# Kernel optimization log

Measured on AMD Instinct MI355X. Metric: run time of the kernel, lower is better.

Reference implementation:

```python
import jax, jax.numpy as jnp
import numpy as np

EPS = 1e-5
B, C_IN, T_IN = 512, 12, 5000
NF, HID, LAT = 32, 64, 32


def setup_inputs() -> dict:
    key = jax.random.key(0)
    ks = jax.random.split(key, 12)
    inp = {
        "x": jax.random.normal(ks[0], (B, C_IN, T_IN), dtype=jnp.float32),
        # conv stack
        "conv1_w": jax.random.normal(ks[1], (32, C_IN, 50), dtype=jnp.float32) * 0.05,
        "conv1_b": jnp.zeros((32,), dtype=jnp.float32),
        "bn1_g": jnp.ones((32,), dtype=jnp.float32),
        "bn1_b": jnp.zeros((32,), dtype=jnp.float32),
        "conv2_w": jax.random.normal(ks[2], (NF, 32, 25), dtype=jnp.float32) * 0.05,
        "conv2_b": jnp.zeros((NF,), dtype=jnp.float32),
        "bn2_g": jnp.ones((NF,), dtype=jnp.float32),
        "bn2_b": jnp.zeros((NF,), dtype=jnp.float32),
        # input projection + layernorm
        "proj_w": jax.random.normal(ks[3], (LAT, NF), dtype=jnp.float32) * 0.1,
        "proj_b": jnp.zeros((LAT,), dtype=jnp.float32),
        "ln_g": jnp.ones((LAT,), dtype=jnp.float32),
        "ln_b": jnp.zeros((LAT,), dtype=jnp.float32),
        # PLRNN recurrence params
        "A": jnp.eye(LAT, dtype=jnp.float32) * 0.9,
        "W": jax.random.normal(ks[4], (LAT, HID), dtype=jnp.float32) * 0.1,
        "h_bias": jnp.zeros((HID,), dtype=jnp.float32),
        # output projection
        "out_w": jax.random.normal(ks[5], (LAT, LAT), dtype=jnp.float32) * 0.1,
        "out_b": jnp.zeros((LAT,), dtype=jnp.float32),
    }
    return inp


def _conv1d(x, w, b, stride):
    # x: [B, C, T], w: [O, I, K]
    y = jax.lax.conv_general_dilated(
        x, w, window_strides=(stride,), padding="VALID",
        dimension_numbers=("NCH", "OIH", "NCH"))
    return y + b[None, :, None]


def _batchnorm_train(x, g, b):
    # training-mode BN over (batch, time) per channel; x: [B, C, T]
    mean = jnp.mean(x, axis=(0, 2), keepdims=True)
    var = jnp.mean((x - mean) ** 2, axis=(0, 2), keepdims=True)
    return (x - mean) * jax.lax.rsqrt(var + EPS) * g[None, :, None] + b[None, :, None]


def _layernorm(x, g, b):
    mean = jnp.mean(x, axis=-1, keepdims=True)
    var = jnp.mean((x - mean) ** 2, axis=-1, keepdims=True)
    return (x - mean) * jax.lax.rsqrt(var + EPS) * g + b


def reference(x, conv1_w, conv1_b, bn1_g, bn1_b, conv2_w, conv2_b, bn2_g, bn2_b,
              proj_w, proj_b, ln_g, ln_b, A, W, h_bias, out_w, out_b):
    # conv front-end
    y = jax.nn.relu(_batchnorm_train(_conv1d(x, conv1_w, conv1_b, 10), bn1_g, bn1_b))
    y = jax.nn.relu(_batchnorm_train(_conv1d(y, conv2_w, conv2_b, 5), bn2_g, bn2_b))
    y = jnp.transpose(y, (0, 2, 1))  # [B, T, NF], T = 95

    # input projection + LN, vectorized over all timesteps
    xt = _layernorm(jnp.einsum("btf,lf->btl", y, proj_w) + proj_b, ln_g, ln_b)  # [B, T, L]
    xs = jnp.transpose(xt, (1, 0, 2))  # [T, B, L] for scan

    def step(h, x_t):
        # h: [B, L]
        linear = h @ A.T
        nonlinear = jax.nn.relu(h @ W + h_bias) @ W.T
        h_new = linear + nonlinear + x_t
        return h_new, h_new

    h0 = jnp.zeros((x.shape[0], A.shape[0]), dtype=x.dtype)
    _, outputs = jax.lax.scan(step, h0, xs)  # [T, B, L]

    pooled = jnp.mean(outputs, axis=0)  # [B, L]
    return pooled @ out_w.T + out_b
```

## Files before the change

### kernel.cpp

```cpp
#include <hip/hip_runtime.h>

#define NB    512
#define CIN   12
#define TIN   5000
#define C1    32
#define T1    496
#define T2    95
#define LATD  32
#define HIDD  64

#define OFS_STATS 0
#define OFS_W1P   256
#define OFS_W2P   19456
#define OFS_Y1    45056
#define OFS_Y2    8171520
#define OFS_XS    OFS_Y1

__global__ void prep_kernel(const float* __restrict__ w1, const float* __restrict__ w2,
                            float* __restrict__ ws) {
    int idx = blockIdx.x * 256 + threadIdx.x;
    if (idx < 256) ws[idx] = 0.f;
    int j = idx - 256;
    if (j >= 0 && j < 19200) {
        int ic = j / 1600, r = j % 1600;
        int p = r / 160, rr = r % 160, jj = rr / 32, oc = rr % 32;
        ws[OFS_W1P + j] = w1[oc * 600 + ic * 50 + 10 * jj + p];
    }
    int j2 = idx - 19456;
    if (j2 >= 0 && j2 < 25600) {
        int ic = j2 / 800, r = j2 % 800;
        int p = r / 160, rr = r % 160, jj = rr / 32, oc = rr % 32;
        ws[OFS_W2P + j2] = w2[oc * 800 + ic * 25 + 5 * jj + p];
    }
}

__global__ __launch_bounds__(256, 4) void conv1_kernel(const float* __restrict__ x,
                                                       const float* __restrict__ b1,
                                                       float* __restrict__ ws) {
    const float* w1p = ws + OFS_W1P;
    float* y1 = ws + OFS_Y1;
    float* stats = ws + OFS_STATS;
    int b  = blockIdx.x >> 1;
    int t0 = (blockIdx.x & 1) * 256;
    int tid = threadIdx.x;
    int ocg = tid & 7, tg = tid >> 3;
    int oc0 = ocg * 4, lt0 = tg * 8;

    __shared__ __align__(16) float xs_s[2][2680];
    __shared__ __align__(16) float ws_s[2][1600];
    __shared__ float sred[256];

    float acc[4][8];
#pragma unroll
    for (int a = 0; a < 4; ++a)
#pragma unroll
        for (int c = 0; c < 8; ++c) acc[a][c] = 0.f;

    const float* xb = x + (size_t)b * (CIN * TIN) + t0 * 10;
    int nvalid = TIN - t0 * 10;

    float4 px[3];
    float4 pw[2];

    auto fetch = [&](int ic) {
#pragma unroll
        for (int j = 0; j < 3; ++j) {
            int i = tid + j * 256;
            if (i < 650) {
                int src = 4 * i;
                const float* gp = xb + ic * TIN + src;
                float4 v;
                if (src + 4 <= nvalid) {
                    v = *(const float4*)gp;
                } else {
                    v.x = (src + 0 < nvalid) ? gp[0] : 0.f;
                    v.y = (src + 1 < nvalid) ? gp[1] : 0.f;
                    v.z = (src + 2 < nvalid) ? gp[2] : 0.f;
                    v.w = (src + 3 < nvalid) ? gp[3] : 0.f;
                }
                px[j] = v;
            }
        }
#pragma unroll
        for (int j = 0; j < 2; ++j) {
            int i = tid + j * 256;
            if (i < 400) pw[j] = *(const float4*)(w1p + ic * 1600 + 4 * i);
        }
    };

    auto stage = [&](int cur) {
#pragma unroll
        for (int j = 0; j < 3; ++j) {
            int i = tid + j * 256;
            if (i < 650) {
                int g = 4 * i;
                int col = g / 10, p = g - 10 * col;
                float vals[4] = {px[j].x, px[j].y, px[j].z, px[j].w};
#pragma unroll
                for (int m = 0; m < 4; ++m) {
                    int pm = p + m;
                    int rr = (pm >= 10) ? pm - 10 : pm;
                    int cc = col + ((pm >= 10) ? 1 : 0);
                    xs_s[cur][rr * 268 + cc] = vals[m];
                }
            }
        }
#pragma unroll
        for (int j = 0; j < 2; ++j) {
            int i = tid + j * 256;
            if (i < 400) *(float4*)&ws_s[cur][4 * i] = pw[j];
        }
    };

    fetch(0);
    stage(0);
    fetch(1);
    __syncthreads();

    for (int ic = 0; ic < CIN; ++ic) {
        int cur = ic & 1;
        if (ic + 1 < CIN) stage(cur ^ 1);
        if (ic + 2 < CIN) fetch(ic + 2);

#pragma unroll 2
        for (int p = 0; p < 10; ++p) {
            const float* xr = &xs_s[cur][p * 268 + 8 * tg];
            float4 xa = *(const float4*)(xr);
            float4 xbv = *(const float4*)(xr + 4);
            float4 xc = *(const float4*)(xr + 8);
            float xv[12] = {xa.x, xa.y, xa.z, xa.w,
                            xbv.x, xbv.y, xbv.z, xbv.w,
                            xc.x, xc.y, xc.z, xc.w};
            const float* wr = &ws_s[cur][p * 160 + oc0];
            float4 w0 = *(const float4*)(wr);
            float4 w1v = *(const float4*)(wr + 32);
            float4 w2v = *(const float4*)(wr + 64);
            float4 w3v = *(const float4*)(wr + 96);
            float4 w4v = *(const float4*)(wr + 128);
            float wj[5][4] = {{w0.x, w0.y, w0.z, w0.w},
                              {w1v.x, w1v.y, w1v.z, w1v.w},
                              {w2v.x, w2v.y, w2v.z, w2v.w},
                              {w3v.x, w3v.y, w3v.z, w3v.w},
                              {w4v.x, w4v.y, w4v.z, w4v.w}};
#pragma unroll
            for (int j = 0; j < 5; ++j)
#pragma unroll
                for (int jt = 0; jt < 8; ++jt) {
                    float xx = xv[jt + j];
#pragma unroll
                    for (int jo = 0; jo < 4; ++jo)
                        acc[jo][jt] = fmaf(wj[j][jo], xx, acc[jo][jt]);
                }
        }
        __syncthreads();
    }

    float bias[4];
#pragma unroll
    for (int jo = 0; jo < 4; ++jo) bias[jo] = b1[oc0 + jo];

    bool tvalid = (t0 + lt0) <= (T1 - 8);
    float psum[4], psq[4];
#pragma unroll
    for (int jo = 0; jo < 4; ++jo) {
        float s = 0.f, q = 0.f;
        if (tvalid) {
            float tmp[8];
#pragma unroll
            for (int jt = 0; jt < 8; ++jt) {
                float v = acc[jo][jt] + bias[jo];
                tmp[jt] = v; s += v; q = fmaf(v, v, q);
            }
            float* yrow = y1 + (size_t)(b * 32 + oc0 + jo) * T1 + t0 + lt0;
            float4 o0; o0.x = tmp[0]; o0.y = tmp[1]; o0.z = tmp[2]; o0.w = tmp[3];
            float4 o1; o1.x = tmp[4]; o1.y = tmp[5]; o1.z = tmp[6]; o1.w = tmp[7];
            *(float4*)yrow       = o0;
            *(float4*)(yrow + 4) = o1;
        }
        psum[jo] = s; psq[jo] = q;
    }
#pragma unroll
    for (int off = 32; off >= 8; off >>= 1) {
#pragma unroll
        for (int jo = 0; jo < 4; ++jo) {
            psum[jo] += __shfl_down(psum[jo], off, 64);
            psq[jo]  += __shfl_down(psq[jo],  off, 64);
        }
    }
    int lane = tid & 63, wvi = tid >> 6;
    if (lane < 8) {
#pragma unroll
        for (int jo = 0; jo < 4; ++jo) {
            sred[((wvi * 8 + lane) * 4 + jo) * 2 + 0] = psum[jo];
            sred[((wvi * 8 + lane) * 4 + jo) * 2 + 1] = psq[jo];
        }
    }
    __syncthreads();
    if (tid < 64) {
        int oc = tid >> 1, which = tid & 1;
        int og = oc >> 2, jo = oc & 3;
        float v = 0.f;
#pragma unroll
        for (int w = 0; w < 4; ++w)
            v += sred[((w * 8 + og) * 4 + jo) * 2 + which];
        atomicAdd(&stats[which * 32 + oc], v);
    }
}

__global__ __launch_bounds__(384, 2) void conv2_kernel(const float* __restrict__ b2,
                                                       const float* __restrict__ g1,
                                                       const float* __restrict__ be1,
                                                       float* __restrict__ ws) {
    const float* w2p = ws + OFS_W2P;
    const float* y1 = ws + OFS_Y1;
    float* y2 = ws + OFS_Y2;
    float* stats = ws + OFS_STATS;
    int b = blockIdx.x;
    int tid = threadIdx.x;
    int hf = (tid >= 192) ? 1 : 0;
    int ltid = tid - hf * 192;
    int icbase = hf * 16;
    int ocg = ltid & 7, tg = ltid >> 3;
    int oc0 = ocg * 4, lt0 = tg * 4;

    __shared__ __align__(16) float a1s[2][2][500];
    __shared__ __align__(16) float w2s[2][2][800];
    __shared__ __align__(16) float comb[16 * 192];
    __shared__ float sred[192];
    __shared__ float bns[64];

    if (tid < 32) {
        float mean = stats[tid] * (1.f / 253952.f);
        float var  = stats[32 + tid] * (1.f / 253952.f) - mean * mean;
        float s = g1[tid] * rsqrtf(var + 1e-5f);
        bns[tid]      = s;
        bns[32 + tid] = be1[tid] - mean * s;
    }

    float acc[4][4];
#pragma unroll
    for (int a = 0; a < 4; ++a)
#pragma unroll
        for (int c = 0; c < 4; ++c) acc[a][c] = 0.f;

    float4 py, pw0, pw1;
    auto fetch = [&](int k) {
        int ic = icbase + k;
        const float* yrow = y1 + (size_t)(b * 32 + ic) * T1;
        if (ltid < 124) py = *(const float4*)(yrow + 4 * ltid);
        pw0 = *(const float4*)(w2p + ic * 800 + 4 * ltid);
        if (ltid < 8) pw1 = *(const float4*)(w2p + ic * 800 + 4 * (ltid + 192));
    };

    auto stage = [&](int k, int cur) {
        int ic = icbase + k;
        if (ltid < 124) {
            float s1 = bns[ic], sh1 = bns[32 + ic];
            float vals[4];
            vals[0] = fmaxf(fmaf(py.x, s1, sh1), 0.f);
            vals[1] = fmaxf(fmaf(py.y, s1, sh1), 0.f);
            vals[2] = fmaxf(fmaf(py.z, s1, sh1), 0.f);
            vals[3] = fmaxf(fmaf(py.w, s1, sh1), 0.f);
            int g = 4 * ltid;
            int col = g / 5, p = g - 5 * col;
#pragma unroll
            for (int m = 0; m < 4; ++m) {
                int pm = p + m;
                int rr = (pm >= 5) ? pm - 5 : pm;
                int cc = col + ((pm >= 5) ? 1 : 0);
                a1s[hf][cur][rr * 100 + cc] = vals[m];
            }
        }
        *(float4*)&w2s[hf][cur][4 * ltid] = pw0;
        if (ltid < 8) *(float4*)&w2s[hf][cur][4 * (ltid + 192)] = pw1;
    };

    fetch(0);
    __syncthreads();
    stage(0, 0);
    fetch(1);
    __syncthreads();

    for (int k = 0; k < 16; ++k) {
        int cur = k & 1;
        if (k + 1 < 16) stage(k + 1, cur ^ 1);
        if (k + 2 < 16) fetch(k + 2);

#pragma unroll 2
        for (int p = 0; p < 5; ++p) {
            const float* xr = &a1s[hf][cur][p * 100 + 4 * tg];
            float4 xa = *(const float4*)(xr);
            float4 xbv = *(const float4*)(xr + 4);
            float xv[8] = {xa.x, xa.y, xa.z, xa.w, xbv.x, xbv.y, xbv.z, xbv.w};
            const float* wr = &w2s[hf][cur][p * 160 + oc0];
            float4 w0 = *(const float4*)(wr);
            float4 w1v = *(const float4*)(wr + 32);
            float4 w2v = *(const float4*)(wr + 64);
            float4 w3v = *(const float4*)(wr + 96);
            float4 w4v = *(const float4*)(wr + 128);
            float wj[5][4] = {{w0.x, w0.y, w0.z, w0.w},
                              {w1v.x, w1v.y, w1v.z, w1v.w},
                              {w2v.x, w2v.y, w2v.z, w2v.w},
                              {w3v.x, w3v.y, w3v.z, w3v.w},
                              {w4v.x, w4v.y, w4v.z, w4v.w}};
#pragma unroll
            for (int j = 0; j < 5; ++j)
#pragma unroll
                for (int jt = 0; jt < 4; ++jt) {
                    float xx = xv[jt + j];
#pragma unroll
                    for (int jo = 0; jo < 4; ++jo)
                        acc[jo][jt] = fmaf(wj[j][jo], xx, acc[jo][jt]);
                }
        }
        __syncthreads();
    }

    if (hf == 1) {
#pragma unroll
        for (int jo = 0; jo < 4; ++jo)
#pragma unroll
            for (int jt = 0; jt < 4; ++jt)
                comb[(jo * 4 + jt) * 192 + ltid] = acc[jo][jt];
    }
    __syncthreads();

    if (hf == 0) {
        float bias[4];
#pragma unroll
        for (int jo = 0; jo < 4; ++jo) bias[jo] = b2[oc0 + jo];

        float psum[4], psq[4];
#pragma unroll
        for (int jo = 0; jo < 4; ++jo) {
            float s = 0.f, q = 0.f;
#pragma unroll
            for (int jt = 0; jt < 4; ++jt) {
                int t2 = lt0 + jt;
                if (t2 < T2) {
                    float v = acc[jo][jt] + comb[(jo * 4 + jt) * 192 + ltid] + bias[jo];
                    y2[(size_t)(b * 32 + oc0 + jo) * T2 + t2] = v;
                    s += v; q = fmaf(v, v, q);
                }
            }
            psum[jo] = s; psq[jo] = q;
        }
#pragma unroll
        for (int off = 32; off >= 8; off >>= 1) {
#pragma unroll
            for (int jo = 0; jo < 4; ++jo) {
                psum[jo] += __shfl_down(psum[jo], off, 64);
                psq[jo]  += __shfl_down(psq[jo],  off, 64);
            }
        }
        int lane = ltid & 63, wvi = ltid >> 6;
        if (lane < 8) {
#pragma unroll
            for (int jo = 0; jo < 4; ++jo) {
                sred[((wvi * 8 + lane) * 4 + jo) * 2 + 0] = psum[jo];
                sred[((wvi * 8 + lane) * 4 + jo) * 2 + 1] = psq[jo];
            }
        }
    }
    __syncthreads();
    if (tid < 64) {
        int oc = tid >> 1, which = tid & 1;
        int og = oc >> 2, jo = oc & 3;
        float v = 0.f;
#pragma unroll
        for (int w = 0; w < 3; ++w)
            v += sred[((w * 8 + og) * 4 + jo) * 2 + which];
        atomicAdd(&stats[64 + which * 32 + oc], v);
    }
}

__global__ __launch_bounds__(256, 2) void proj_kernel(const float* __restrict__ g2,
                                                      const float* __restrict__ be2,
                                                      const float* __restrict__ pw,
                                                      const float* __restrict__ pb,
                                                      const float* __restrict__ lng,
                                                      const float* __restrict__ lnb,
                                                      float* __restrict__ ws) {
    int b = blockIdx.x;
    int tid = threadIdx.x;
    __shared__ float a2s[3040];
    __shared__ float pws[1056];
    __shared__ float bns2[64];
    const float* stats = ws + OFS_STATS;
    const float* y2 = ws + OFS_Y2 + (size_t)b * (32 * T2);
    float* xsg = ws + OFS_XS;

    if (tid < 32) {
        float mean = stats[64 + tid] * (1.f / 48640.f);
        float var  = stats[96 + tid] * (1.f / 48640.f) - mean * mean;
        float s = g2[tid] * rsqrtf(var + 1e-5f);
        bns2[tid]      = s;
        bns2[32 + tid] = be2[tid] - mean * s;
    }
    __syncthreads();

    for (int i = tid; i < 3040; i += 256) {
        int f = i / 95;
        a2s[i] = fmaxf(fmaf(y2[i], bns2[f], bns2[32 + f]), 0.f);
    }
    for (int i = tid; i < 1024; i += 256)
        pws[(i >> 5) * 33 + (i & 31)] = pw[i];

    int l = tid & 31, ts = tid >> 5;
    float pbv = pb[l], lg = lng[l], lb = lnb[l];
    __syncthreads();

    for (int it = 0; it < 12; ++it) {
        int t = ts + 8 * it;
        if (t < T2) {
            float v = pbv;
#pragma unroll
            for (int f = 0; f < 32; ++f)
                v = fmaf(a2s[f * T2 + t], pws[l * 33 + f], v);
            float sum = v;
#pragma unroll
            for (int off = 16; off >= 1; off >>= 1) sum += __shfl_xor(sum, off, 64);
            float mean = sum * (1.f / 32.f);
            float d = v - mean;
            float q = d * d;
#pragma unroll
            for (int off = 16; off >= 1; off >>= 1) q += __shfl_xor(q, off, 64);
            float o = d * rsqrtf(q * (1.f / 32.f) + 1e-5f) * lg + lb;
            xsg[(size_t)t * (NB * 32) + b * 32 + l] = o;
        }
    }
}

__global__ __launch_bounds__(64)
__attribute__((amdgpu_waves_per_eu(1, 1)))
void scan_kernel(const float* __restrict__ Am,
                 const float* __restrict__ Wm,
                 const float* __restrict__ hbp,
                 const float* __restrict__ ow,
                 const float* __restrict__ ob,
                 const float* __restrict__ ws,
                 float* __restrict__ out) {
    int b = blockIdx.x;
    int lane = threadIdx.x;
    int l = lane & 31, half = lane >> 5;
    __shared__ __align__(16) float hs[32];
    __shared__ __align__(16) float hds[64];
    __shared__ float ows[1056];

    float Wc[32], WT[32], Ah[16];
#pragma unroll
    for (int j = 0; j < 32; ++j) Wc[j] = Wm[j * HIDD + lane];
#pragma unroll
    for (int m = 0; m < 32; ++m) WT[m] = Wm[l * HIDD + half * 32 + m];
#pragma unroll
    for (int j = 0; j < 16; ++j) Ah[j] = Am[l * 32 + half * 16 + j];
    float hbv = hbp[lane];
    for (int i = lane; i < 1024; i += 64)
        ows[(i >> 5) * 33 + (i & 31)] = ow[i];

    const float* xsg = ws + OFS_XS + b * 32;
    if (lane < 32) hs[l] = 0.f;
    float xv = xsg[l];
    float pool = 0.f;
    __syncthreads();

    for (int t = 0; t < T2; ++t) {
        __syncthreads();
        float4 hv[8];
#pragma unroll
        for (int q = 0; q < 8; ++q) hv[q] = *(const float4*)&hs[4 * q];
        float a0 = hbv, a1 = 0.f, a2 = 0.f, a3 = 0.f;
#pragma unroll
        for (int q = 0; q < 8; ++q) {
            a0 = fmaf(Wc[4 * q + 0], hv[q].x, a0);
            a1 = fmaf(Wc[4 * q + 1], hv[q].y, a1);
            a2 = fmaf(Wc[4 * q + 2], hv[q].z, a2);
            a3 = fmaf(Wc[4 * q + 3], hv[q].w, a3);
        }
        float hid = fmaxf((a0 + a1) + (a2 + a3), 0.f);
        float4 hl[4];
#pragma unroll
        for (int q = 0; q < 4; ++q) hl[q] = *(const float4*)&hs[half * 16 + 4 * q];
        float l0 = 0.f, l1 = 0.f;
#pragma unroll
        for (int q = 0; q < 4; ++q) {
            l0 = fmaf(Ah[4 * q + 0], hl[q].x, l0);
            l1 = fmaf(Ah[4 * q + 1], hl[q].y, l1);
            l0 = fmaf(Ah[4 * q + 2], hl[q].z, l0);
            l1 = fmaf(Ah[4 * q + 3], hl[q].w, l1);
        }
        float lin = l0 + l1;
        hds[lane] = hid;
        __syncthreads();
        float n0 = 0.f, n1 = 0.f, n2 = 0.f, n3 = 0.f;
#pragma unroll
        for (int q = 0; q < 8; ++q) {
            float4 d4 = *(const float4*)&hds[half * 32 + 4 * q];
            n0 = fmaf(WT[4 * q + 0], d4.x, n0);
            n1 = fmaf(WT[4 * q + 1], d4.y, n1);
            n2 = fmaf(WT[4 * q + 2], d4.z, n2);
            n3 = fmaf(WT[4 * q + 3], d4.w, n3);
        }
        float part = (n0 + n1) + (n2 + n3) + lin;
        part += __shfl_xor(part, 32, 64);
        float hnew = part + xv;
        pool += hnew;
        if (t + 1 < T2) xv = xsg[(size_t)(t + 1) * (NB * 32) + l];
        if (lane < 32) hs[l] = hnew;
    }

    __syncthreads();
    if (lane < 32) hs[l] = pool * (1.f / 95.f);
    __syncthreads();
    if (lane < 32) {
        float4 p0 = *(const float4*)&hs[0];
        float4 p1 = *(const float4*)&hs[4];
        float4 p2 = *(const float4*)&hs[8];
        float4 p3 = *(const float4*)&hs[12];
        float4 p4 = *(const float4*)&hs[16];
        float4 p5 = *(const float4*)&hs[20];
        float4 p6 = *(const float4*)&hs[24];
        float4 p7 = *(const float4*)&hs[28];
        float o = ob[l];
        const float* owr = &ows[l * 33];
        o = fmaf(owr[0],  p0.x, o); o = fmaf(owr[1],  p0.y, o);
        o = fmaf(owr[2],  p0.z, o); o = fmaf(owr[3],  p0.w, o);
        o = fmaf(owr[4],  p1.x, o); o = fmaf(owr[5],  p1.y, o);
        o = fmaf(owr[6],  p1.z, o); o = fmaf(owr[7],  p1.w, o);
        o = fmaf(owr[8],  p2.x, o); o = fmaf(owr[9],  p2.y, o);
        o = fmaf(owr[10], p2.z, o); o = fmaf(owr[11], p2.w, o);
        o = fmaf(owr[12], p3.x, o); o = fmaf(owr[13], p3.y, o);
        o = fmaf(owr[14], p3.z, o); o = fmaf(owr[15], p3.w, o);
        o = fmaf(owr[16], p4.x, o); o = fmaf(owr[17], p4.y, o);
        o = fmaf(owr[18], p4.z, o); o = fmaf(owr[19], p4.w, o);
        o = fmaf(owr[20], p5.x, o); o = fmaf(owr[21], p5.y, o);
        o = fmaf(owr[22], p5.z, o); o = fmaf(owr[23], p5.w, o);
        o = fmaf(owr[24], p6.x, o); o = fmaf(owr[25], p6.y, o);
        o = fmaf(owr[26], p6.z, o); o = fmaf(owr[27], p6.w, o);
        o = fmaf(owr[28], p7.x, o); o = fmaf(owr[29], p7.y, o);
        o = fmaf(owr[30], p7.z, o); o = fmaf(owr[31], p7.w, o);
        out[b * 32 + l] = o;
    }
}

extern "C" void kernel_launch(void* const* d_in, const int* in_sizes, int n_in,
                              void* d_out, int out_size, void* d_ws, size_t ws_size,
                              hipStream_t stream) {
    (void)in_sizes; (void)n_in; (void)out_size; (void)ws_size;
    const float* x   = (const float*)d_in[0];
    const float* w1  = (const float*)d_in[1];
    const float* b1  = (const float*)d_in[2];
    const float* g1  = (const float*)d_in[3];
    const float* be1 = (const float*)d_in[4];
    const float* w2  = (const float*)d_in[5];
    const float* b2  = (const float*)d_in[6];
    const float* g2  = (const float*)d_in[7];
    const float* be2 = (const float*)d_in[8];
    const float* pw  = (const float*)d_in[9];
    const float* pb  = (const float*)d_in[10];
    const float* lng = (const float*)d_in[11];
    const float* lnb = (const float*)d_in[12];
    const float* Am  = (const float*)d_in[13];
    const float* Wm  = (const float*)d_in[14];
    const float* hb  = (const float*)d_in[15];
    const float* ow  = (const float*)d_in[16];
    const float* ob  = (const float*)d_in[17];
    float* ws  = (float*)d_ws;
    float* out = (float*)d_out;

    prep_kernel<<<176, 256, 0, stream>>>(w1, w2, ws);
    conv1_kernel<<<1024, 256, 0, stream>>>(x, b1, ws);
    conv2_kernel<<<512, 384, 0, stream>>>(b2, g1, be1, ws);
    proj_kernel<<<512, 256, 0, stream>>>(g2, be2, pw, pb, lng, lnb, ws);
    scan_kernel<<<512, 64, 0, stream>>>(Am, Wm, hb, ow, ob, ws, out);
}
```

Before: 402.7 us.

## Fuse projection/layernorm into scan kernel and drop intra-wave barriers

Merges the projection+layernorm kernel with the recurrent scan kernel so the normalized inputs stay in shared memory instead of being written to and re-read from global memory, which also removes one kernel launch. After the projection phase, only the first 64-thread wave runs the recurrence, and the per-step __syncthreads are removed because a single wave executes in lockstep. The cost is that 192 threads per block sit idle during the serial scan, and the shared-memory footprint per block grows. Correctness of the barrier removal relies on in-order LDS access within one wave rather than on an explicit fence.

Measured after the change: 405.6 us. No clear change (+0.7%).

```diff
diff --git a/kernel.cpp b/kernel.cpp
--- a/kernel.cpp
+++ b/kernel.cpp
@@ -14,7 +14,6 @@
 #define OFS_W2P   19456
 #define OFS_Y1    45056
 #define OFS_Y2    8171520
-#define OFS_XS    OFS_Y1
 
 __global__ void prep_kernel(const float* __restrict__ w1, const float* __restrict__ w2,
                             float* __restrict__ ws) {
@@ -374,21 +373,26 @@
     }
 }
 
-__global__ __launch_bounds__(256, 2) void proj_kernel(const float* __restrict__ g2,
-                                                      const float* __restrict__ be2,
-                                                      const float* __restrict__ pw,
-                                                      const float* __restrict__ pb,
-                                                      const float* __restrict__ lng,
-                                                      const float* __restrict__ lnb,
-                                                      float* __restrict__ ws) {
+__global__ __launch_bounds__(256, 2) void projscan_kernel(
+    const float* __restrict__ g2,  const float* __restrict__ be2,
+    const float* __restrict__ pw,  const float* __restrict__ pb,
+    const float* __restrict__ lng, const float* __restrict__ lnb,
+    const float* __restrict__ Am,  const float* __restrict__ Wm,
+    const float* __restrict__ hbp, const float* __restrict__ ow,
+    const float* __restrict__ ob,  const float* __restrict__ ws,
+    float* __restrict__ out) {
     int b = blockIdx.x;
     int tid = threadIdx.x;
     __shared__ float a2s[3040];
     __shared__ float pws[1056];
     __shared__ float bns2[64];
+    __shared__ __align__(16) float xsl[95 * 32];
+    __shared__ float ows[1056];
+    __shared__ __align__(16) float hs[32];
+    __shared__ __align__(16) float hds[64];
+
     const float* stats = ws + OFS_STATS;
     const float* y2 = ws + OFS_Y2 + (size_t)b * (32 * T2);
-    float* xsg = ws + OFS_XS;
 
     if (tid < 32) {
         float mean = stats[64 + tid] * (1.f / 48640.f);
@@ -403,8 +407,10 @@
         int f = i / 95;
         a2s[i] = fmaxf(fmaf(y2[i], bns2[f], bns2[32 + f]), 0.f);
     }
-    for (int i = tid; i < 1024; i += 256)
+    for (int i = tid; i < 1024; i += 256) {
         pws[(i >> 5) * 33 + (i & 31)] = pw[i];
+        ows[(i >> 5) * 33 + (i & 31)] = ow[i];
+    }
 
     int l = tid & 31, ts = tid >> 5;
     float pbv = pb[l], lg = lng[l], lb = lnb[l];
@@ -425,27 +431,14 @@
             float q = d * d;
 #pragma unroll
             for (int off = 16; off >= 1; off >>= 1) q += __shfl_xor(q, off, 64);
-            float o = d * rsqrtf(q * (1.f / 32.f) + 1e-5f) * lg + lb;
-            xsg[(size_t)t * (NB * 32) + b * 32 + l] = o;
-        }
-    }
-}
-
-__global__ __launch_bounds__(64)
-__attribute__((amdgpu_waves_per_eu(1, 1)))
-void scan_kernel(const float* __restrict__ Am,
-                 const float* __restrict__ Wm,
-                 const float* __restrict__ hbp,
-                 const float* __restrict__ ow,
-                 const float* __restrict__ ob,
-                 const float* __restrict__ ws,
-                 float* __restrict__ out) {
-    int b = blockIdx.x;
-    int lane = threadIdx.x;
-    int l = lane & 31, half = lane >> 5;
-    __shared__ __align__(16) float hs[32];
-    __shared__ __align__(16) float hds[64];
-    __shared__ float ows[1056];
+            xsl[t * 32 + l] = d * rsqrtf(q * (1.f / 32.f) + 1e-5f) * lg + lb;
+        }
+    }
+    __syncthreads();
+    if (tid >= 64) return;
+
+    int lane = tid;
+    int half = lane >> 5;
 
     float Wc[32], WT[32], Ah[16];
 #pragma unroll
@@ -455,17 +448,12 @@
 #pragma unroll
     for (int j = 0; j < 16; ++j) Ah[j] = Am[l * 32 + half * 16 + j];
     float hbv = hbp[lane];
-    for (int i = lane; i < 1024; i += 64)
-        ows[(i >> 5) * 33 + (i & 31)] = ow[i];
-
-    const float* xsg = ws + OFS_XS + b * 32;
+
     if (lane < 32) hs[l] = 0.f;
-    float xv = xsg[l];
+    float xv = xsl[l];
     float pool = 0.f;
-    __syncthreads();
 
     for (int t = 0; t < T2; ++t) {
-        __syncthreads();
         float4 hv[8];
 #pragma unroll
         for (int q = 0; q < 8; ++q) hv[q] = *(const float4*)&hs[4 * q];
@@ -491,7 +479,6 @@
         }
         float lin = l0 + l1;
         hds[lane] = hid;
-        __syncthreads();
         float n0 = 0.f, n1 = 0.f, n2 = 0.f, n3 = 0.f;
 #pragma unroll
         for (int q = 0; q < 8; ++q) {
@@ -505,13 +492,11 @@
         part += __shfl_xor(part, 32, 64);
         float hnew = part + xv;
         pool += hnew;
-        if (t + 1 < T2) xv = xsg[(size_t)(t + 1) * (NB * 32) + l];
+        if (t + 1 < T2) xv = xsl[(t + 1) * 32 + l];
         if (lane < 32) hs[l] = hnew;
     }
 
-    __syncthreads();
     if (lane < 32) hs[l] = pool * (1.f / 95.f);
-    __syncthreads();
     if (lane < 32) {
         float4 p0 = *(const float4*)&hs[0];
         float4 p1 = *(const float4*)&hs[4];
@@ -571,6 +556,6 @@
     prep_kernel<<<176, 256, 0, stream>>>(w1, w2, ws);
     conv1_kernel<<<1024, 256, 0, stream>>>(x, b1, ws);
     conv2_kernel<<<512, 384, 0, stream>>>(b2, g1, be1, ws);
-    proj_kernel<<<512, 256, 0, stream>>>(g2, be2, pw, pb, lng, lnb, ws);
-    scan_kernel<<<512, 64, 0, stream>>>(Am, Wm, hb, ow, ob, ws, out);
+    projscan_kernel<<<512, 256, 0, stream>>>(g2, be2, pw, pb, lng, lnb,
+                                             Am, Wm, hb, ow, ob, ws, out);
 }
```
